# Kernel optimization log

Hardware: AMD Instinct MI355X
Metric: run time of the kernel (lower is better)

Reference implementation:

```python
import jax, jax.numpy as jnp
import numpy as np

V = 30522   # vocab / node count
A = 2       # num adjacency matrices
H = 128     # hid_dim
O = 16      # out_dim
B = 8       # batch
D = 256     # doc/sequence dim
NNZ = 250000  # nonzeros per adjacency


def setup_inputs() -> dict:
    key = jax.random.key(0)
    k = jax.random.split(key, 7)
    x_dv = jax.random.normal(k[0], (B, D, V), jnp.float32)
    adj_rows = jax.random.randint(k[1], (A, NNZ), 0, V)
    adj_cols = jax.random.randint(k[2], (A, NNZ), 0, V)
    adj_vals = jax.random.uniform(k[3], (A, NNZ), jnp.float32)
    W_vh = jax.random.normal(k[4], (A, V, H), jnp.float32) * 0.02
    fc_W = jax.random.normal(k[5], (H, O), jnp.float32) * 0.05
    fc_b = jnp.zeros((O,), jnp.float32)
    return {"x_dv": x_dv, "adj_rows": adj_rows, "adj_cols": adj_cols,
            "adj_vals": adj_vals, "W_vh": W_vh, "fc_W": fc_W, "fc_b": fc_b}


def reference(x_dv, adj_rows, adj_cols, adj_vals, W_vh, fc_W, fc_b):
    # Per-adjacency sparse mm: h_vh[a] = A_a @ W_a, A_a in COO form. [A, V, H]
    def spmm(rows, cols, vals, W):
        # gather rows of W at cols, scale by vals, scatter-add into output rows
        return jax.ops.segment_sum(vals[:, None] * W[cols], rows, num_segments=V)

    h_vh = jax.vmap(spmm)(adj_rows, adj_cols, adj_vals, W_vh)  # [A, V, H]
    # Dropout is identity in eval mode. fused_h = sum_a x_dv @ h_vh[a]
    # = x_dv @ sum_a h_vh[a] (x_dv is shared across adjacencies).
    h_sum = h_vh.sum(axis=0)                                   # [V, H]
    fused_h = jnp.einsum('bdv,vh->bdh', x_dv, h_sum)           # [B, D, H]
    return fused_h @ fc_W + fc_b                               # [B, D, O]
```

## Files before the change

### kernel.cpp

```cpp
#include <hip/hip_runtime.h>

#define V_N 30522
#define A_N 2
#define H_N 128
#define O_N 16
#define NNZ_N 250000
#define NNZ_T (A_N * NNZ_N)
#define M_N 2048
#define AV_N (A_N * V_N)

#define KPAD 30720
#define KSPL 64
#define KC (KPAD / KSPL)
#define NCHUNK 30
#define PADW (KPAD - V_N)

typedef __attribute__((ext_vector_type(8))) short bf16x8_t;
typedef __attribute__((ext_vector_type(4))) float f32x4_t;

static __device__ __forceinline__ unsigned short f2bf(float f) {
    union { float f; unsigned u; } v; v.f = f;
    unsigned r = v.u + 0x7fffu + ((v.u >> 16) & 1u);
    return (unsigned short)(r >> 16);
}

__global__ __launch_bounds__(256) void wfc_kernel(const float* __restrict__ W,
                                                  const float* __restrict__ fcW,
                                                  float* __restrict__ wfc,
                                                  int* __restrict__ count) {
    int gtid = blockIdx.x * 256 + threadIdx.x;
    if (gtid < V_N) count[gtid] = 0;

    __shared__ float wrow[16][128];
    int row0 = blockIdx.x * 16;
    for (int idx = threadIdx.x; idx < 16 * 32; idx += 256) {
        int r = idx >> 5, c4 = (idx & 31) * 4;
        int grow = row0 + r;
        float4 v = make_float4(0.f, 0.f, 0.f, 0.f);
        if (grow < AV_N)
            v = *reinterpret_cast<const float4*>(W + (size_t)grow * H_N + c4);
        *reinterpret_cast<float4*>(&wrow[r][c4]) = v;
    }
    __syncthreads();
    int r = threadIdx.x >> 4, o = threadIdx.x & 15;
    int grow = row0 + r;
    if (grow >= AV_N) return;
    float s = 0.f;
#pragma unroll
    for (int h = 0; h < H_N; ++h) s += wrow[r][h] * fcW[h * O_N + o];
    wfc[(size_t)grow * O_N + o] = s;
}

__global__ __launch_bounds__(256) void hist_kernel(const int* __restrict__ rows,
                                                   int* __restrict__ count,
                                                   short* __restrict__ hw_t) {
    int n = blockIdx.x * blockDim.x + threadIdx.x;
    if (n < O_N * PADW) {
        int o = n / PADW, v2 = V_N + (n - o * PADW);
        hw_t[(size_t)o * KPAD + v2] = 0;
    }
    if (n >= NNZ_T) return;
    atomicAdd(&count[rows[n]], 1);
}

__global__ __launch_bounds__(1024) void scanA_kernel(const int* __restrict__ count,
                                                     int* __restrict__ csum) {
    __shared__ int sdata[1024];
    int tid = threadIdx.x;
    int i = blockIdx.x * 1024 + tid;
    sdata[tid] = (i < V_N) ? count[i] : 0;
    __syncthreads();
    for (int off = 512; off > 0; off >>= 1) {
        if (tid < off) sdata[tid] += sdata[tid + off];
        __syncthreads();
    }
    if (tid == 0) csum[blockIdx.x] = sdata[0];
}

__global__ __launch_bounds__(1024) void scanC_kernel(const int* __restrict__ count,
                                                     const int* __restrict__ csum,
                                                     int* __restrict__ row_start,
                                                     int* __restrict__ cursor) {
    __shared__ int sdata[1024];
    __shared__ int coff_s;
    int tid = threadIdx.x;
    int bid = blockIdx.x;
    if (tid < 32) {
        int own = (tid < NCHUNK) ? csum[tid] : 0;
        int v = own;
#pragma unroll
        for (int d = 1; d < 32; d <<= 1) {
            int t = __shfl_up(v, d, 32);
            if (tid >= d) v += t;
        }
        if (tid == bid) coff_s = v - own;
        if (bid == 0 && tid == NCHUNK - 1) row_start[V_N] = v;
    }
    int i = bid * 1024 + tid;
    int v = (i < V_N) ? count[i] : 0;
    sdata[tid] = v;
    __syncthreads();
    for (int off = 1; off < 1024; off <<= 1) {
        int t = (tid >= off) ? sdata[tid - off] : 0;
        __syncthreads();
        sdata[tid] += t;
        __syncthreads();
    }
    int exc = sdata[tid] - v + coff_s;
    if (i < V_N) { row_start[i] = exc; cursor[i] = exc; }
}

__global__ __launch_bounds__(256) void scatter_kernel(const int* __restrict__ rows,
                                                      const int* __restrict__ cols,
                                                      const float* __restrict__ vals,
                                                      int* __restrict__ cursor,
                                                      unsigned long long* __restrict__ scv) {
    int n = blockIdx.x * blockDim.x + threadIdx.x;
    if (n >= NNZ_T) return;
    int a = (n >= NNZ_N) ? 1 : 0;
    int r = rows[n];
    int pos = atomicAdd(&cursor[r], 1);
    union { float f; unsigned u; } uv; uv.f = vals[n];
    scv[pos] = ((unsigned long long)uv.u << 32) | (unsigned)(a * V_N + cols[n]);
}

__global__ __launch_bounds__(256) void accum_hw_kernel(const int* __restrict__ row_start,
                                                       const unsigned long long* __restrict__ scv,
                                                       const float* __restrict__ wfc,
                                                       short* __restrict__ hw_t) {
    int gid = blockIdx.x * blockDim.x + threadIdx.x;
    if (gid >= V_N * O_N) return;
    int row = gid >> 4, o = gid & 15;
    int s = row_start[row];
    int e = row_start[row + 1];
    float acc = 0.f;
    for (int i = s; i < e; ++i) {
        unsigned long long cv = scv[i];
        int cp = (int)(cv & 0xffffffffu);
        union { unsigned u; float f; } uv; uv.u = (unsigned)(cv >> 32);
        acc += uv.f * wfc[(size_t)cp * O_N + o];
    }
    hw_t[(size_t)o * KPAD + row] = (short)f2bf(acc);
}

__global__ __launch_bounds__(256) void gemm_mfma5(const float* __restrict__ X,
                                                  const short* __restrict__ hw_t,
                                                  float* __restrict__ partials) {
    const int tid = threadIdx.x;
    const int w = tid >> 6;
    const int lane = tid & 63;
    const int l15 = lane & 15;
    const int kg = lane >> 4;
    const int row0 = blockIdx.x * 64 + w * 16;
    const int by = blockIdx.y;
    const int k0 = by * KC;

    const float* xrow = X + (size_t)(row0 + l15) * V_N;
    const short* hrow = hw_t + (size_t)l15 * KPAD;

    f32x4_t acc = {};

#pragma unroll 2
    for (int kb = k0; kb < k0 + KC; kb += 32) {
        int k = kb + kg * 8;
        float a[8];
        if (k + 7 < V_N) {
            const float2* p = reinterpret_cast<const float2*>(xrow + k);
            float2 u0 = p[0], u1 = p[1], u2 = p[2], u3 = p[3];
            a[0] = u0.x; a[1] = u0.y; a[2] = u1.x; a[3] = u1.y;
            a[4] = u2.x; a[5] = u2.y; a[6] = u3.x; a[7] = u3.y;
        } else {
#pragma unroll
            for (int j = 0; j < 8; ++j) a[j] = (k + j < V_N) ? xrow[k + j] : 0.f;
        }
        bf16x8_t av;
#pragma unroll
        for (int j = 0; j < 8; ++j) av[j] = (short)f2bf(a[j]);
        bf16x8_t bv = *reinterpret_cast<const bf16x8_t*>(hrow + k);
        acc = __builtin_amdgcn_mfma_f32_16x16x32_bf16(av, bv, acc, 0, 0, 0);
    }

#pragma unroll
    for (int r4 = 0; r4 < 4; ++r4)
        partials[((size_t)by * M_N + row0 + kg * 4 + r4) * O_N + l15] = acc[r4];
}

__global__ __launch_bounds__(256) void reduce_kernel(const float* __restrict__ partials,
                                                     const float* __restrict__ fcb,
                                                     float* __restrict__ out) {
    int idx = blockIdx.x * 256 + threadIdx.x;
    if (idx >= M_N * O_N) return;
    float s = fcb[idx & 15];
#pragma unroll
    for (int by = 0; by < KSPL; ++by)
        s += partials[(size_t)by * M_N * O_N + idx];
    out[idx] = s;
}

extern "C" void kernel_launch(void* const* d_in, const int* in_sizes, int n_in,
                              void* d_out, int out_size, void* d_ws, size_t ws_size,
                              hipStream_t stream) {
    const float* x    = (const float*)d_in[0];
    const int* rows   = (const int*)d_in[1];
    const int* cols   = (const int*)d_in[2];
    const float* vals = (const float*)d_in[3];
    const float* W    = (const float*)d_in[4];
    const float* fcW  = (const float*)d_in[5];
    const float* fcb  = (const float*)d_in[6];
    float* out = (float*)d_out;

    char* base = (char*)d_ws;
    size_t off = 0;
    auto alloc = [&](size_t bytes) { size_t p = off; off = (off + bytes + 255) & ~(size_t)255; return p; };
    size_t o_wfc    = alloc((size_t)AV_N * O_N * 4);
    size_t o_hwt    = alloc((size_t)O_N * KPAD * 2);
    size_t o_count  = alloc((size_t)V_N * 4);
    size_t o_rstart = alloc((size_t)(V_N + 1) * 4);
    size_t o_cursor = alloc((size_t)V_N * 4);
    size_t o_scv    = alloc((size_t)NNZ_T * 8);
    size_t o_csum   = alloc((size_t)NCHUNK * 4);
    size_t o_part   = alloc((size_t)KSPL * M_N * O_N * 4);

    float* wfc        = (float*)(base + o_wfc);
    short* hw_t       = (short*)(base + o_hwt);
    int*   count      = (int*)(base + o_count);
    int*   row_start  = (int*)(base + o_rstart);
    int*   cursor     = (int*)(base + o_cursor);
    unsigned long long* scv = (unsigned long long*)(base + o_scv);
    int*   csum       = (int*)(base + o_csum);
    float* partials   = (float*)(base + o_part);

    wfc_kernel<<<(AV_N + 15) / 16, 256, 0, stream>>>(W, fcW, wfc, count);
    hist_kernel<<<(NNZ_T + 255) / 256, 256, 0, stream>>>(rows, count, hw_t);
    scanA_kernel<<<NCHUNK, 1024, 0, stream>>>(count, csum);
    scanC_kernel<<<NCHUNK, 1024, 0, stream>>>(count, csum, row_start, cursor);
    scatter_kernel<<<(NNZ_T + 255) / 256, 256, 0, stream>>>(rows, cols, vals, cursor, scv);
    accum_hw_kernel<<<(V_N * O_N + 255) / 256, 256, 0, stream>>>(row_start, scv, wfc, hw_t);

    gemm_mfma5<<<dim3(M_N / 64, KSPL), 256, 0, stream>>>(x, hw_t, partials);
    reduce_kernel<<<(M_N * O_N + 255) / 256, 256, 0, stream>>>(partials, fcb, out);
}
```

Before: 181.0 us.

## Stage X tiles through LDS with coalesced float4 loads and register prefetch

The GEMM kernel now loads 128-column slabs of X with row-contiguous float4 loads into padded shared memory, prefetching the next slab into registers while MFMAs consume the current one. Each wave reads back only the rows it wrote itself, so no barrier is needed. The K split drops from 64 to 30, which gives longer per-block loops and fewer partial sums to reduce. The last K chunk, which runs past V, keeps the old direct-load path. The aim is better coalescing and latency hiding on the bandwidth-bound X read, at the cost of LDS use and extra registers.

Result: slower. 234.2 us (+29.4%).

```diff
diff --git a/kernel.cpp b/kernel.cpp
--- a/kernel.cpp
+++ b/kernel.cpp
@@ -10,8 +10,10 @@
 #define AV_N (A_N * V_N)
 
 #define KPAD 30720
-#define KSPL 64
+#define KSPL 30
 #define KC (KPAD / KSPL)
+#define NMEGA 8
+#define PADB 528
 #define NCHUNK 30
 #define PADW (KPAD - V_N)
 
@@ -143,7 +145,7 @@
     hw_t[(size_t)o * KPAD + row] = (short)f2bf(acc);
 }
 
-__global__ __launch_bounds__(256) void gemm_mfma5(const float* __restrict__ X,
+__global__ __launch_bounds__(256) void gemm_mfma6(const float* __restrict__ X,
                                                   const short* __restrict__ hw_t,
                                                   float* __restrict__ partials) {
     const int tid = threadIdx.x;
@@ -151,38 +153,84 @@
     const int lane = tid & 63;
     const int l15 = lane & 15;
     const int kg = lane >> 4;
-    const int row0 = blockIdx.x * 64 + w * 16;
+    const int bx = blockIdx.x;
     const int by = blockIdx.y;
+    const int row0 = bx * 64;
     const int k0 = by * KC;
 
-    const float* xrow = X + (size_t)(row0 + l15) * V_N;
-    const short* hrow = hw_t + (size_t)l15 * KPAD;
+    __shared__ __align__(16) char xs[64 * PADB];
 
     f32x4_t acc = {};
 
+    if (k0 + KC <= V_N) {
+        const int lrow = lane >> 5;
+        const int lcol = (lane & 31) * 16;
+        const int q0 = w * 8;
+        float4 r[8];
+
+        auto LOADM = [&](int mg) {
+#pragma unroll
+            for (int q = 0; q < 8; ++q) {
+                int i = (q0 + q) * 2 + lrow;
+                const char* src = (const char*)X +
+                    ((size_t)(row0 + i) * V_N + (size_t)(k0 + mg * 128)) * 4 + lcol;
+                r[q] = *reinterpret_cast<const float4*>(src);
+            }
+        };
+        auto DSW = [&]() {
+#pragma unroll
+            for (int q = 0; q < 8; ++q) {
+                int i = (q0 + q) * 2 + lrow;
+                *reinterpret_cast<float4*>(xs + i * PADB + lcol) = r[q];
+            }
+        };
+
+        LOADM(0);
+        const char* arow = xs + (w * 16 + l15) * PADB;
+        for (int mg = 0; mg < NMEGA; ++mg) {
+            DSW();
+            if (mg + 1 < NMEGA) LOADM(mg + 1);
+            const short* hk = hw_t + (size_t)l15 * KPAD + k0 + mg * 128;
+#pragma unroll
+            for (int s = 0; s < 4; ++s) {
+                const float4 f0 = *reinterpret_cast<const float4*>(arow + s * 128 + kg * 32);
+                const float4 f1 = *reinterpret_cast<const float4*>(arow + s * 128 + kg * 32 + 16);
+                bf16x8_t av;
+                av[0] = (short)f2bf(f0.x); av[1] = (short)f2bf(f0.y);
+                av[2] = (short)f2bf(f0.z); av[3] = (short)f2bf(f0.w);
+                av[4] = (short)f2bf(f1.x); av[5] = (short)f2bf(f1.y);
+                av[6] = (short)f2bf(f1.z); av[7] = (short)f2bf(f1.w);
+                bf16x8_t bv = *reinterpret_cast<const bf16x8_t*>(hk + s * 32 + kg * 8);
+                acc = __builtin_amdgcn_mfma_f32_16x16x32_bf16(av, bv, acc, 0, 0, 0);
+            }
+        }
+    } else {
+        const float* xrow = X + (size_t)(row0 + w * 16 + l15) * V_N;
+        const short* hrow = hw_t + (size_t)l15 * KPAD;
 #pragma unroll 2
-    for (int kb = k0; kb < k0 + KC; kb += 32) {
-        int k = kb + kg * 8;
-        float a[8];
-        if (k + 7 < V_N) {
-            const float2* p = reinterpret_cast<const float2*>(xrow + k);
-            float2 u0 = p[0], u1 = p[1], u2 = p[2], u3 = p[3];
-            a[0] = u0.x; a[1] = u0.y; a[2] = u1.x; a[3] = u1.y;
-            a[4] = u2.x; a[5] = u2.y; a[6] = u3.x; a[7] = u3.y;
-        } else {
-#pragma unroll
-            for (int j = 0; j < 8; ++j) a[j] = (k + j < V_N) ? xrow[k + j] : 0.f;
+        for (int kb = k0; kb < k0 + KC; kb += 32) {
+            int k = kb + kg * 8;
+            float a[8];
+            if (k + 7 < V_N) {
+                const float2* p = reinterpret_cast<const float2*>(xrow + k);
+                float2 u0 = p[0], u1 = p[1], u2 = p[2], u3 = p[3];
+                a[0] = u0.x; a[1] = u0.y; a[2] = u1.x; a[3] = u1.y;
+                a[4] = u2.x; a[5] = u2.y; a[6] = u3.x; a[7] = u3.y;
+            } else {
+#pragma unroll
+                for (int j = 0; j < 8; ++j) a[j] = (k + j < V_N) ? xrow[k + j] : 0.f;
+            }
+            bf16x8_t av;
+#pragma unroll
+            for (int j = 0; j < 8; ++j) av[j] = (short)f2bf(a[j]);
+            bf16x8_t bv = *reinterpret_cast<const bf16x8_t*>(hrow + k);
+            acc = __builtin_amdgcn_mfma_f32_16x16x32_bf16(av, bv, acc, 0, 0, 0);
         }
-        bf16x8_t av;
-#pragma unroll
-        for (int j = 0; j < 8; ++j) av[j] = (short)f2bf(a[j]);
-        bf16x8_t bv = *reinterpret_cast<const bf16x8_t*>(hrow + k);
-        acc = __builtin_amdgcn_mfma_f32_16x16x32_bf16(av, bv, acc, 0, 0, 0);
     }
 
 #pragma unroll
     for (int r4 = 0; r4 < 4; ++r4)
-        partials[((size_t)by * M_N + row0 + kg * 4 + r4) * O_N + l15] = acc[r4];
+        partials[((size_t)by * M_N + row0 + w * 16 + kg * 4 + r4) * O_N + l15] = acc[r4];
 }
 
 __global__ __launch_bounds__(256) void reduce_kernel(const float* __restrict__ partials,
@@ -237,6 +285,6 @@
     scatter_kernel<<<(NNZ_T + 255) / 256, 256, 0, stream>>>(rows, cols, vals, cursor, scv);
     accum_hw_kernel<<<(V_N * O_N + 255) / 256, 256, 0, stream>>>(row_start, scv, wfc, hw_t);
 
-    gemm_mfma5<<<dim3(M_N / 64, KSPL), 256, 0, stream>>>(x, hw_t, partials);
+    gemm_mfma6<<<dim3(M_N / 64, KSPL), 256, 0, stream>>>(x, hw_t, partials);
     reduce_kernel<<<(M_N * O_N + 255) / 256, 256, 0, stream>>>(partials, fcb, out);
 }
```

## Replace MFMA skinny GEMM with VALU FMA kernel on k-major bf16 weights

Applied to the files above, without the earlier changes.

Replaces the bf16 MFMA GEMM of X[2048x30522] by hw[30522x16] with a plain FP32 VALU kernel. The hw matrix is transposed to k-major layout so each lane reads 16 outputs per k contiguously. Each 64-lane block handles 4 rows and one of 8 k-splits, then reduces across lanes with shuffles. This removes the X-to-bf16 conversion and cuts partial sums from 64 to 8 splits. The cost is many more FMA instructions and a long shuffle reduction, on a GEMM that is bound by reading X from memory.

After: 220.3 us. +21.7%, slower.

```diff
diff --git a/kernel.cpp b/kernel.cpp
--- a/kernel.cpp
+++ b/kernel.cpp
@@ -10,18 +10,26 @@
 #define AV_N (A_N * V_N)
 
 #define KPAD 30720
-#define KSPL 64
-#define KC (KPAD / KSPL)
 #define NCHUNK 30
-#define PADW (KPAD - V_N)
+#define PADN ((KPAD - V_N) * O_N)
+
+#define RB 4
+#define VKS 8
+#define VKC (KPAD / VKS)
+#define VITER (VKC / 256)
 
 typedef __attribute__((ext_vector_type(8))) short bf16x8_t;
-typedef __attribute__((ext_vector_type(4))) float f32x4_t;
 
 static __device__ __forceinline__ unsigned short f2bf(float f) {
     union { float f; unsigned u; } v; v.f = f;
     unsigned r = v.u + 0x7fffu + ((v.u >> 16) & 1u);
     return (unsigned short)(r >> 16);
+}
+
+static __device__ __forceinline__ float bf2f(short s) {
+    union { unsigned u; float f; } v;
+    v.u = ((unsigned)(unsigned short)s) << 16;
+    return v.f;
 }
 
 __global__ __launch_bounds__(256) void wfc_kernel(const float* __restrict__ W,
@@ -53,12 +61,9 @@
 
 __global__ __launch_bounds__(256) void hist_kernel(const int* __restrict__ rows,
                                                    int* __restrict__ count,
-                                                   short* __restrict__ hw_t) {
+                                                   short* __restrict__ hw_kt) {
     int n = blockIdx.x * blockDim.x + threadIdx.x;
-    if (n < O_N * PADW) {
-        int o = n / PADW, v2 = V_N + (n - o * PADW);
-        hw_t[(size_t)o * KPAD + v2] = 0;
-    }
+    if (n < PADN) hw_kt[(size_t)V_N * O_N + n] = 0;
     if (n >= NNZ_T) return;
     atomicAdd(&count[rows[n]], 1);
 }
@@ -127,7 +132,7 @@
 __global__ __launch_bounds__(256) void accum_hw_kernel(const int* __restrict__ row_start,
                                                        const unsigned long long* __restrict__ scv,
                                                        const float* __restrict__ wfc,
-                                                       short* __restrict__ hw_t) {
+                                                       short* __restrict__ hw_kt) {
     int gid = blockIdx.x * blockDim.x + threadIdx.x;
     if (gid >= V_N * O_N) return;
     int row = gid >> 4, o = gid & 15;
@@ -140,49 +145,76 @@
         union { unsigned u; float f; } uv; uv.u = (unsigned)(cv >> 32);
         acc += uv.f * wfc[(size_t)cp * O_N + o];
     }
-    hw_t[(size_t)o * KPAD + row] = (short)f2bf(acc);
-}
-
-__global__ __launch_bounds__(256) void gemm_mfma5(const float* __restrict__ X,
-                                                  const short* __restrict__ hw_t,
-                                                  float* __restrict__ partials) {
-    const int tid = threadIdx.x;
-    const int w = tid >> 6;
-    const int lane = tid & 63;
-    const int l15 = lane & 15;
-    const int kg = lane >> 4;
-    const int row0 = blockIdx.x * 64 + w * 16;
-    const int by = blockIdx.y;
-    const int k0 = by * KC;
-
-    const float* xrow = X + (size_t)(row0 + l15) * V_N;
-    const short* hrow = hw_t + (size_t)l15 * KPAD;
-
-    f32x4_t acc = {};
-
-#pragma unroll 2
-    for (int kb = k0; kb < k0 + KC; kb += 32) {
-        int k = kb + kg * 8;
-        float a[8];
-        if (k + 7 < V_N) {
-            const float2* p = reinterpret_cast<const float2*>(xrow + k);
-            float2 u0 = p[0], u1 = p[1], u2 = p[2], u3 = p[3];
-            a[0] = u0.x; a[1] = u0.y; a[2] = u1.x; a[3] = u1.y;
-            a[4] = u2.x; a[5] = u2.y; a[6] = u3.x; a[7] = u3.y;
+    hw_kt[(size_t)row * O_N + o] = (short)f2bf(acc);
+}
+
+__global__ __launch_bounds__(64) void gemm_valu(const float* __restrict__ X,
+                                                const short* __restrict__ hw_kt,
+                                                float* __restrict__ partials) {
+    const int lane = threadIdx.x;
+    const int rg = blockIdx.x;
+    const int ks = blockIdx.y;
+    const int row0 = rg * RB;
+    const int kbase = ks * VKC + lane * 4;
+
+    float acc[RB][16];
+#pragma unroll
+    for (int r = 0; r < RB; ++r)
+#pragma unroll
+        for (int o = 0; o < 16; ++o) acc[r][o] = 0.f;
+
+    for (int it = 0; it < VITER; ++it) {
+        const int k = kbase + it * 256;
+        float xv[RB][4];
+        if (k + 3 < V_N) {
+#pragma unroll
+            for (int r = 0; r < RB; ++r) {
+                const float2* p = reinterpret_cast<const float2*>(X + (size_t)(row0 + r) * V_N + k);
+                float2 u0 = p[0], u1 = p[1];
+                xv[r][0] = u0.x; xv[r][1] = u0.y; xv[r][2] = u1.x; xv[r][3] = u1.y;
+            }
         } else {
 #pragma unroll
-            for (int j = 0; j < 8; ++j) a[j] = (k + j < V_N) ? xrow[k + j] : 0.f;
-        }
-        bf16x8_t av;
-#pragma unroll
-        for (int j = 0; j < 8; ++j) av[j] = (short)f2bf(a[j]);
-        bf16x8_t bv = *reinterpret_cast<const bf16x8_t*>(hrow + k);
-        acc = __builtin_amdgcn_mfma_f32_16x16x32_bf16(av, bv, acc, 0, 0, 0);
-    }
-
-#pragma unroll
-    for (int r4 = 0; r4 < 4; ++r4)
-        partials[((size_t)by * M_N + row0 + kg * 4 + r4) * O_N + l15] = acc[r4];
+            for (int r = 0; r < RB; ++r)
+#pragma unroll
+                for (int j = 0; j < 4; ++j)
+                    xv[r][j] = (k + j < V_N) ? X[(size_t)(row0 + r) * V_N + k + j] : 0.f;
+        }
+        const short* hp = hw_kt + (size_t)k * O_N;
+        bf16x8_t hv[8];
+#pragma unroll
+        for (int q = 0; q < 8; ++q) hv[q] = *reinterpret_cast<const bf16x8_t*>(hp + q * 8);
+#pragma unroll
+        for (int j = 0; j < 4; ++j) {
+            float hwf[16];
+#pragma unroll
+            for (int i = 0; i < 8; ++i) {
+                hwf[i] = bf2f(hv[2 * j][i]);
+                hwf[8 + i] = bf2f(hv[2 * j + 1][i]);
+            }
+#pragma unroll
+            for (int r = 0; r < RB; ++r) {
+                float xs = xv[r][j];
+#pragma unroll
+                for (int o = 0; o < 16; ++o) acc[r][o] += xs * hwf[o];
+            }
+        }
+    }
+
+#pragma unroll
+    for (int r = 0; r < RB; ++r)
+#pragma unroll
+        for (int o = 0; o < 16; ++o) {
+            float v = acc[r][o];
+#pragma unroll
+            for (int d = 1; d < 64; d <<= 1) v += __shfl_xor(v, d, 64);
+            acc[r][o] = v;
+        }
+    if (lane < 16) {
+#pragma unroll
+        for (int r = 0; r < RB; ++r)
+            partials[((size_t)ks * M_N + row0 + r) * O_N + lane] = acc[r][lane];
+    }
 }
 
 __global__ __launch_bounds__(256) void reduce_kernel(const float* __restrict__ partials,
@@ -192,8 +224,8 @@
     if (idx >= M_N * O_N) return;
     float s = fcb[idx & 15];
 #pragma unroll
-    for (int by = 0; by < KSPL; ++by)
-        s += partials[(size_t)by * M_N * O_N + idx];
+    for (int ks = 0; ks < VKS; ++ks)
+        s += partials[(size_t)ks * M_N * O_N + idx];
     out[idx] = s;
 }
 
@@ -213,16 +245,16 @@
     size_t off = 0;
     auto alloc = [&](size_t bytes) { size_t p = off; off = (off + bytes + 255) & ~(size_t)255; return p; };
     size_t o_wfc    = alloc((size_t)AV_N * O_N * 4);
-    size_t o_hwt    = alloc((size_t)O_N * KPAD * 2);
+    size_t o_hwt    = alloc((size_t)KPAD * O_N * 2);
     size_t o_count  = alloc((size_t)V_N * 4);
     size_t o_rstart = alloc((size_t)(V_N + 1) * 4);
     size_t o_cursor = alloc((size_t)V_N * 4);
     size_t o_scv    = alloc((size_t)NNZ_T * 8);
     size_t o_csum   = alloc((size_t)NCHUNK * 4);
-    size_t o_part   = alloc((size_t)KSPL * M_N * O_N * 4);
+    size_t o_part   = alloc((size_t)VKS * M_N * O_N * 4);
 
     float* wfc        = (float*)(base + o_wfc);
-    short* hw_t       = (short*)(base + o_hwt);
+    short* hw_kt      = (short*)(base + o_hwt);
     int*   count      = (int*)(base + o_count);
     int*   row_start  = (int*)(base + o_rstart);
     int*   cursor     = (int*)(base + o_cursor);
@@ -231,12 +263,12 @@
     float* partials   = (float*)(base + o_part);
 
     wfc_kernel<<<(AV_N + 15) / 16, 256, 0, stream>>>(W, fcW, wfc, count);
-    hist_kernel<<<(NNZ_T + 255) / 256, 256, 0, stream>>>(rows, count, hw_t);
+    hist_kernel<<<(NNZ_T + 255) / 256, 256, 0, stream>>>(rows, count, hw_kt);
     scanA_kernel<<<NCHUNK, 1024, 0, stream>>>(count, csum);
     scanC_kernel<<<NCHUNK, 1024, 0, stream>>>(count, csum, row_start, cursor);
     scatter_kernel<<<(NNZ_T + 255) / 256, 256, 0, stream>>>(rows, cols, vals, cursor, scv);
-    accum_hw_kernel<<<(V_N * O_N + 255) / 256, 256, 0, stream>>>(row_start, scv, wfc, hw_t);
-
-    gemm_mfma5<<<dim3(M_N / 64, KSPL), 256, 0, stream>>>(x, hw_t, partials);
+    accum_hw_kernel<<<(V_N * O_N + 255) / 256, 256, 0, stream>>>(row_start, scv, wfc, hw_kt);
+
+    gemm_valu<<<dim3(M_N / RB, VKS), 64, 0, stream>>>(x, hw_kt, partials);
     reduce_kernel<<<(M_N * O_N + 255) / 256, 256, 0, stream>>>(partials, fcb, out);
 }
```
